# Optimization experiments

Hardware: AMD Instinct MI355X
Metric: run time of the kernel (lower is better)

## Reference

```python
import jax, jax.numpy as jnp
import numpy as np

B, CIN, COUT = 4, 256, 256
H, W = 48, 48
KH = KW = 7
SH = SW = 1
PH = PW = 3
REL = COUT // 2  # rel_size with groups=1


def setup_inputs() -> dict:
    key = jax.random.key(0)
    ks = jax.random.split(key, 7)
    fan = float(CIN)
    x = jax.random.normal(ks[0], (B, CIN, H, W), jnp.float32)
    w_q = jax.random.normal(ks[1], (COUT, CIN), jnp.float32) * (2.0 / fan) ** 0.5
    w_k = jax.random.normal(ks[2], (COUT, CIN), jnp.float32) * (2.0 / fan) ** 0.5
    w_v = jax.random.normal(ks[3], (COUT, CIN), jnp.float32) * (2.0 / fan) ** 0.5
    bound = 1.0 / np.sqrt(COUT)
    bias = jax.random.uniform(ks[4], (1, COUT, 1, 1), jnp.float32, -bound, bound)
    rel_x = jax.random.normal(ks[5], (REL, KW), jnp.float32)
    rel_y = jax.random.normal(ks[6], (COUT - REL, KH), jnp.float32)
    return {"x": x, "w_q": w_q, "w_k": w_k, "w_v": w_v, "bias": bias,
            "rel_x": rel_x, "rel_y": rel_y}


def reference(x, w_q, w_k, w_v, bias, rel_x, rel_y):
    b = x.shape[0]
    ph, pw = H + 2 * PH, W + 2 * PW
    fh = (ph - KH) // SH + 1
    fw = (pw - KW) // SW + 1
    xp = jnp.pad(x, ((0, 0), (0, 0), (PH, PH), (PW, PW)))
    # 1x1 convs (groups=1) as channel matmuls
    vq = jnp.einsum('oc,bchw->bohw', w_q, xp)
    vk = jnp.einsum('oc,bchw->bohw', w_k, xp)
    vv = jnp.einsum('oc,bchw->bohw', w_v, xp)
    # query at window centers: [b, C, fh, fw]
    win_q = vq[:, :, (KH - 1) // 2: ph - KH // 2: SH, (KW - 1) // 2: pw - KW // 2: SW]
    # relative position terms (sum over channel halves)
    qx = jnp.einsum('bxhw,xk->bhwk', win_q[:, :REL], rel_x)        # [b,fh,fw,kw]
    qy = jnp.einsum('byhw,yk->bhwk', win_q[:, REL:], rel_y)        # [b,fh,fw,kh]
    # overlapping windows via gather (equivalent to torch unfold)
    I = jnp.arange(fh)[:, None] * SH + jnp.arange(KH)[None, :]     # [fh,kh]
    J = jnp.arange(fw)[:, None] * SW + jnp.arange(KW)[None, :]     # [fw,kw]
    win_k = vk[:, :, I[:, None, :, None], J[None, :, None, :]]     # [b,C,fh,fw,kh,kw]
    # channel-summed attention logits (shared across channels, as in source)
    scores = jnp.einsum('bchw,bchwkl->bhwkl', win_q, win_k)
    scores = scores + qy[:, :, :, :, None] + qx[:, :, :, None, :]
    attn = jax.nn.softmax(scores.reshape(b, fh, fw, KH * KW), axis=-1)
    attn = attn.reshape(b, fh, fw, KH, KW)
    win_v = vv[:, :, I[:, None, :, None], J[None, :, None, :]]     # [b,C,fh,fw,kh,kw]
    out = jnp.einsum('bhwkl,bchwkl->bchw', attn, win_v) + bias
    return out
```

## Files before the change

kernel.cpp:

```cpp
#include <hip/hip_runtime.h>

#define BB 4
#define CC 256
#define HH 48
#define WW 48
#define HWHW 2304
#define KK 49
#define RELN 128

#define QSZ (BB*CC*HWHW)
#define ATTNOFF (3*QSZ)
#define SBUF_FLOATS (BB*HH*64*WW)
#define WTOFF (ATTNOFF + SBUF_FLOATS)
#define WT_FLOATS 196608
#define KBOFF (WTOFF + WT_FLOATS)
#define KB_FLOATS 3145728
#define RBOFF (KBOFF + KB_FLOATS)

typedef short bf16x8 __attribute__((ext_vector_type(8)));
typedef float f32x4 __attribute__((ext_vector_type(4)));

__device__ __forceinline__ void split_bf16(float f, unsigned short& hi, unsigned short& lo)
{
    unsigned u = __float_as_uint(f);
    hi = (unsigned short)(u >> 16);
    float r = f - __uint_as_float(u & 0xFFFF0000u);
    unsigned v = __float_as_uint(r);
    v += 0x7FFFu + ((v >> 16) & 1u);
    lo = (unsigned short)(v >> 16);
}

__device__ __forceinline__ void gload16(const uint4* g, uint4* l)
{
    __builtin_amdgcn_global_load_lds(
        (const __attribute__((address_space(1))) void*)g,
        (__attribute__((address_space(3))) void*)l, 16, 0, 0);
}

__global__ __launch_bounds__(256) void prep_kernel(
    const float* __restrict__ x,
    const float* __restrict__ wq, const float* __restrict__ wk,
    const float* __restrict__ wvp,
    const float* __restrict__ relx, const float* __restrict__ rely,
    unsigned short* __restrict__ xt, unsigned short* __restrict__ wt,
    float* __restrict__ ws)
{
    __shared__ unsigned short lds[32*520];
    const int bid = blockIdx.x;
    const int t = threadIdx.x;

    if (bid < 288) {
        const int b = bid / 72;
        const int hw0 = (bid % 72) * 32;
        const int hw = t & 31, cp = t >> 5;
        #pragma unroll 4
        for (int i = 0; i < 32; ++i) {
            int c = i*8 + cp;
            float f = x[((size_t)b*CC + c)*HWHW + hw0 + hw];
            unsigned short hi, lo; split_bf16(f, hi, lo);
            int ch = i*2;
            lds[hw*520 + ((ch       ^ (hw&7))*8) + cp] = hi;
            lds[hw*520 + (((ch + 1) ^ (hw&7))*8) + cp] = lo;
        }
        __syncthreads();
        const int hw2 = t >> 3, u = t & 7;
        uint4* xt4 = (uint4*)xt;
        const size_t rowbase = ((size_t)b*HWHW + hw0 + hw2) * 64;
        #pragma unroll
        for (int j = 0; j < 8; ++j) {
            int chunk = j*8 + u;
            uint4 v = *(const uint4*)&lds[hw2*520 + chunk*8];
            xt4[rowbase + chunk] = v;
        }
        return;
    }
    if (bid < 384) {
        const int tt = (bid - 288)*256 + t;
        const int m = tt >> 5, kg = tt & 31;
        const float* src = (m < 256) ? wq : (m < 512) ? wk : wvp;
        const float* row = src + (size_t)(m & 255)*256 + kg*8;
        unsigned short h[8], l[8];
        #pragma unroll
        for (int j = 0; j < 8; ++j) split_bf16(row[j], h[j], l[j]);
        uint4 hv, lv;
        hv.x = (unsigned)h[0] | ((unsigned)h[1]<<16); hv.y = (unsigned)h[2] | ((unsigned)h[3]<<16);
        hv.z = (unsigned)h[4] | ((unsigned)h[5]<<16); hv.w = (unsigned)h[6] | ((unsigned)h[7]<<16);
        lv.x = (unsigned)l[0] | ((unsigned)l[1]<<16); lv.y = (unsigned)l[2] | ((unsigned)l[3]<<16);
        lv.z = (unsigned)l[4] | ((unsigned)l[5]<<16); lv.w = (unsigned)l[6] | ((unsigned)l[7]<<16);
        uint4* dstrow = (uint4*)wt + (size_t)m*64;
        const int ks = kg >> 2, s_hi = 2*(kg & 3);
        dstrow[ks*8 + ( s_hi      ^ (m&7))] = hv;
        dstrow[ks*8 + ((s_hi + 1) ^ (m&7))] = lv;
        return;
    }
    if (bid < 576) {
        uint4* kb4 = (uint4*)(ws + KBOFF);
        const uint4 z = make_uint4(0u,0u,0u,0u);
        int u0 = (bid - 384)*256 + t;
        #pragma unroll
        for (int it = 0; it < 4; ++it) {
            int u = u0 + it*49152;
            int bch = u >> 7, rem = u & 127;
            int r16 = rem >> 3, gr = rem & 7;
            int r = (r16 < 3) ? r16 : 48 + r16;
            kb4[((size_t)bch*64 + r)*8 + gr] = z;
        }
        return;
    }
    {
        unsigned short* rb = (unsigned short*)(ws + RBOFF);
        #pragma unroll
        for (int it = 0; it < 4; ++it) {
            int idx = t + it*256;
            int gi  = idx & 7;
            int l   = (idx >> 3) & 15;
            int ck4 = (idx >> 7) & 3;
            int rel = idx >> 9;
            int isLo = gi >> 2, g4i = gi & 3;
            unsigned short vals[8];
            #pragma unroll
            for (int j = 0; j < 8; ++j) {
                int cl = ck4*32 + g4i*8 + j;
                float f = (l < 7) ? (rel ? rely[cl*7 + l] : relx[cl*7 + l]) : 0.f;
                unsigned short hi, lo; split_bf16(f, hi, lo);
                vals[j] = isLo ? lo : hi;
            }
            int slot = gi ^ (l & 7);
            unsigned short* dst = rb + (((size_t)rel*4 + ck4)*16 + l)*64 + slot*8;
            uint4 pack;
            pack.x = (unsigned)vals[0] | ((unsigned)vals[1]<<16);
            pack.y = (unsigned)vals[2] | ((unsigned)vals[3]<<16);
            pack.z = (unsigned)vals[4] | ((unsigned)vals[5]<<16);
            pack.w = (unsigned)vals[6] | ((unsigned)vals[7]<<16);
            *(uint4*)dst = pack;
        }
    }
}

__global__ __launch_bounds__(256) void proj_gemm_kernel(
    const unsigned short* __restrict__ xt,
    const unsigned short* __restrict__ wt,
    float* __restrict__ ws)
{
    __shared__ uint4 smem[2][1024];
    const int n0 = blockIdx.x * 64;
    const int m0 = blockIdx.y * 64;
    const int b = n0 / HWHW;
    const int hwb = n0 % HWHW;
    const int tid = threadIdx.x;
    const int wid = tid >> 6, ln = tid & 63;
    const int wm = wid >> 1, wn = wid & 1;
    const int l15 = ln & 15, g = ln >> 4;

    f32x4 acc[2][2];
    #pragma unroll
    for (int i = 0; i < 2; ++i)
        #pragma unroll
        for (int j = 0; j < 2; ++j) acc[i][j] = (f32x4){0.f,0.f,0.f,0.f};

    const uint4* wt4 = (const uint4*)wt;
    const uint4* xt4 = (const uint4*)xt;
    const int lrow = ln >> 3, lslot = ln & 7;

    #define STAGE(bf, ks)                                                          \
        {                                                                          \
            _Pragma("unroll")                                                      \
            for (int i = 0; i < 2; ++i) {                                          \
                int seg = wid*2 + i;                                               \
                int row = seg*8 + lrow;                                            \
                gload16(wt4 + (size_t)(m0 + row)*64 + (ks)*8 + lslot,              \
                        &smem[bf][seg*64]);                                        \
                gload16(xt4 + (size_t)(n0 + row)*64 + (ks)*8 + lslot,              \
                        &smem[bf][512 + seg*64]);                                  \
            }                                                                      \
        }

    STAGE(0, 0);
    #pragma unroll
    for (int ks = 0; ks < 8; ++ks) {
        const int cur = ks & 1;
        if (ks < 7) STAGE(cur ^ 1, ks + 1);
        if (ks < 7) asm volatile("s_waitcnt vmcnt(4)" ::: "memory");
        else        asm volatile("s_waitcnt vmcnt(0)" ::: "memory");
        __builtin_amdgcn_s_barrier();
        __builtin_amdgcn_sched_barrier(0);
        bf16x8 aH[2], aL[2], bH[2], bL[2];
        #pragma unroll
        for (int mt = 0; mt < 2; ++mt) {
            int rA = wm*32 + mt*16 + l15;
            aH[mt] = *(const bf16x8*)&smem[cur][rA*8 + ((2*g)   ^ (rA&7))];
            aL[mt] = *(const bf16x8*)&smem[cur][rA*8 + ((2*g+1) ^ (rA&7))];
        }
        #pragma unroll
        for (int nt = 0; nt < 2; ++nt) {
            int rB = wn*32 + nt*16 + l15;
            bH[nt] = *(const bf16x8*)&smem[cur][512 + rB*8 + ((2*g)   ^ (rB&7))];
            bL[nt] = *(const bf16x8*)&smem[cur][512 + rB*8 + ((2*g+1) ^ (rB&7))];
        }
        #pragma unroll
        for (int mt = 0; mt < 2; ++mt)
            #pragma unroll
            for (int nt = 0; nt < 2; ++nt) {
                acc[mt][nt] = __builtin_amdgcn_mfma_f32_16x16x32_bf16(aH[mt], bH[nt], acc[mt][nt], 0, 0, 0);
                acc[mt][nt] = __builtin_amdgcn_mfma_f32_16x16x32_bf16(aH[mt], bL[nt], acc[mt][nt], 0, 0, 0);
                acc[mt][nt] = __builtin_amdgcn_mfma_f32_16x16x32_bf16(aL[mt], bH[nt], acc[mt][nt], 0, 0, 0);
            }
        if (ks < 7) {
            asm volatile("s_waitcnt lgkmcnt(0)" ::: "memory");
            __builtin_amdgcn_s_barrier();
        }
    }
    #undef STAGE

    const int proj = m0 >> 8;
    if (proj == 2) {
        #pragma unroll
        for (int mt = 0; mt < 2; ++mt) {
            int chb = (m0 & 255) + wm*32 + mt*16 + 4*g;
            int ch4 = chb >> 2;
            #pragma unroll
            for (int nt = 0; nt < 2; ++nt) {
                int hw = hwb + wn*32 + nt*16 + l15;
                float* dst = ws + (size_t)2*QSZ + (((size_t)b*64 + ch4)*HWHW + hw)*4;
                *(f32x4*)dst = acc[mt][nt];
            }
        }
        return;
    }
    __syncthreads();
    unsigned short* eb = (unsigned short*)&smem[0][0];
    #pragma unroll
    for (int mt = 0; mt < 2; ++mt) {
        const int chb = (m0 & 255) + wm*32 + mt*16 + 4*g;
        const int ckl = (chb >> 5) & 1;
        const int p = chb & 31, g8 = p >> 3, half = (p >> 2) & 1;
        #pragma unroll
        for (int nt = 0; nt < 2; ++nt) {
            const int hwl = wn*32 + nt*16 + l15;
            const int w = (hwb + hwl) % 48;
            const int key = (proj == 0 ? w : w + 3) & 7;
            f32x4 v = acc[mt][nt];
            unsigned short h0,h1,h2,h3,q0,q1,q2,q3;
            split_bf16(v[0],h0,q0); split_bf16(v[1],h1,q1);
            split_bf16(v[2],h2,q2); split_bf16(v[3],h3,q3);
            uint2 hv, lv;
            hv.x = (unsigned)h0 | ((unsigned)h1<<16); hv.y = (unsigned)h2 | ((unsigned)h3<<16);
            lv.x = (unsigned)q0 | ((unsigned)q1<<16); lv.y = (unsigned)q2 | ((unsigned)q3<<16);
            const int base = (ckl*64 + hwl)*64;
            *(uint2*)(eb + base + ((g8 ^ key)*8 + half*4))     = hv;
            *(uint2*)(eb + base + (((g8+4) ^ key)*8 + half*4)) = lv;
        }
    }
    __syncthreads();
    const int ck0 = (m0 & 255) >> 5;
    if (proj == 0) {
        const uint4* src = (const uint4*)eb;
        uint4* qb4 = (uint4*)ws;
        #pragma unroll
        for (int ckl2 = 0; ckl2 < 2; ++ckl2) {
            uint4* dst = qb4 + (((size_t)b*8 + ck0 + ckl2)*HWHW + hwb)*8;
            #pragma unroll
            for (int it = 0; it < 2; ++it)
                dst[tid + it*256] = src[ckl2*512 + tid + it*256];
        }
    } else {
        uint4* kb4 = (uint4*)(ws + KBOFF);
        const uint4* src = (const uint4*)eb;
        #pragma unroll
        for (int it = 0; it < 4; ++it) {
            int u = tid + it*256;
            int row = u >> 3, gr = u & 7;
            int ckl2 = row >> 6, hwl2 = row & 63;
            int hw2 = hwb + hwl2, h2 = hw2/48, w2 = hw2%48;
            uint4* dst = kb4 + ((((size_t)b*8 + ck0 + ckl2)*48 + h2)*64 + (w2+3))*8;
            dst[gr] = src[u];
        }
    }
}

__global__ __launch_bounds__(512) void scores2_kernel(float* __restrict__ ws)
{
    __shared__ unsigned short sAll[2][4096*8];
    __shared__ float sc[63][48];

    const int bid = blockIdx.x;
    const int b = bid / 48, h = bid % 48;
    const int tid = threadIdx.x;
    const int wv = tid >> 6, ln = tid & 63;
    const int l15 = ln & 15, g4 = ln >> 4;
    const int key = l15 & 7;

    const unsigned short* QB = (const unsigned short*)ws;
    const unsigned short* KB = (const unsigned short*)(ws + KBOFF);
    const unsigned short* RB = (const unsigned short*)(ws + RBOFF);

    for (int u = tid; u < 63*48; u += 512) ((float*)sc)[u] = 0.f;

    const int dk = wv;
    const int hp = h + dk - 3;
    const bool dok = (wv < 7) && (hp >= 0) && (hp < 48);

    f32x4 acc[6], qx[3], qy[3];
    #pragma unroll
    for (int i = 0; i < 6; ++i) acc[i] = (f32x4){0.f,0.f,0.f,0.f};
    #pragma unroll
    for (int i = 0; i < 3; ++i) { qx[i] = (f32x4){0.f,0.f,0.f,0.f}; qy[i] = (f32x4){0.f,0.f,0.f,0.f}; }

    #define SSTAGE(bf, ck)                                                         \
        {                                                                          \
            _Pragma("unroll")                                                      \
            for (int e = 0; e < 8; ++e) {                                          \
                const int I = wv*8 + e;                                            \
                uint4* dst = (uint4*)sAll[bf] + I*64;                              \
                if (I < 6) {                                                       \
                    int unit = I*64 + ln; int row = unit >> 3, gr = unit & 7;      \
                    gload16((const uint4*)QB                                       \
                        + ((((size_t)b*8 + (ck))*48 + h)*48 + row)*8 + gr, dst);   \
                } else if (I < 62) {                                               \
                    int uk = (I-6)*64 + ln;                                        \
                    int kri = uk >> 9;                                             \
                    int wi = uk & 511; int row = wi >> 3, gr = wi & 7;             \
                    int kh = h + kri - 3;                                          \
                    int khc = kh < 0 ? 0 : (kh > 47 ? 47 : kh);                    \
                    gload16((const uint4*)KB                                       \
                        + ((((size_t)b*8 + (ck))*48 + khc)*64 + row)*8 + gr, dst); \
                } else {                                                           \
                    int ur = (I-62)*64 + ln; int row = ur >> 3, gr = ur & 7;       \
                    int rel = (ck) >> 2, c4 = (ck) & 3;                            \
                    gload16((const uint4*)RB                                       \
                        + (((size_t)rel*4 + c4)*16 + row)*8 + gr, dst);            \
                }                                                                  \
            }                                                                      \
        }

    SSTAGE(0, 0);
    for (int ck = 0; ck < 8; ++ck) {
        const int cur = ck & 1;
        if (ck < 7) SSTAGE(cur ^ 1, ck + 1);
        if (ck < 7) asm volatile("s_waitcnt vmcnt(8)" ::: "memory");
        else        asm volatile("s_waitcnt vmcnt(0)" ::: "memory");
        __builtin_amdgcn_s_barrier();
        __builtin_amdgcn_sched_barrier(0);

        const unsigned short* sQ = sAll[cur];
        const unsigned short* sK = sAll[cur] + 384*8;
        const unsigned short* sR = sAll[cur] + 3968*8;

        bf16x8 AH[3], AL[3];
        #pragma unroll
        for (int i = 0; i < 3; ++i) {
            const unsigned short* qr = sQ + (16*i + l15)*64;
            AH[i] = *(const bf16x8*)(qr + ((g4       ^ key)*8));
            AL[i] = *(const bf16x8*)(qr + (((g4 + 4) ^ key)*8));
        }

        if (wv < 7) {
            if (dok) {
                const unsigned short* kbase = sK + dk*4096;
                bf16x8 BH[4], BL[4];
                #pragma unroll
                for (int j = 0; j < 4; ++j) {
                    const unsigned short* kr = kbase + (j*16 + l15)*64;
                    BH[j] = *(const bf16x8*)(kr + ((g4       ^ key)*8));
                    BL[j] = *(const bf16x8*)(kr + (((g4 + 4) ^ key)*8));
                }
                #pragma unroll
                for (int i = 0; i < 3; ++i) {
                    acc[i*2]   = __builtin_amdgcn_mfma_f32_16x16x32_bf16(AH[i], BH[i],   acc[i*2],   0,0,0);
                    acc[i*2]   = __builtin_amdgcn_mfma_f32_16x16x32_bf16(AH[i], BL[i],   acc[i*2],   0,0,0);
                    acc[i*2]   = __builtin_amdgcn_mfma_f32_16x16x32_bf16(AL[i], BH[i],   acc[i*2],   0,0,0);
                    acc[i*2+1] = __builtin_amdgcn_mfma_f32_16x16x32_bf16(AH[i], BH[i+1], acc[i*2+1], 0,0,0);
                    acc[i*2+1] = __builtin_amdgcn_mfma_f32_16x16x32_bf16(AH[i], BL[i+1], acc[i*2+1], 0,0,0);
                    acc[i*2+1] = __builtin_amdgcn_mfma_f32_16x16x32_bf16(AL[i], BH[i+1], acc[i*2+1], 0,0,0);
                }
            }
        } else {
            const unsigned short* rr = sR + l15*64;
            bf16x8 RH = *(const bf16x8*)(rr + ((g4       ^ key)*8));
            bf16x8 RL = *(const bf16x8*)(rr + (((g4 + 4) ^ key)*8));
            if (ck < 4) {
                #pragma unroll
                for (int i = 0; i < 3; ++i) {
                    qx[i] = __builtin_amdgcn_mfma_f32_16x16x32_bf16(AH[i], RH, qx[i], 0,0,0);
                    qx[i] = __builtin_amdgcn_mfma_f32_16x16x32_bf16(AH[i], RL, qx[i], 0,0,0);
                    qx[i] = __builtin_amdgcn_mfma_f32_16x16x32_bf16(AL[i], RH, qx[i], 0,0,0);
                }
            } else {
                #pragma unroll
                for (int i = 0; i < 3; ++i) {
                    qy[i] = __builtin_amdgcn_mfma_f32_16x16x32_bf16(AH[i], RH, qy[i], 0,0,0);
                    qy[i] = __builtin_amdgcn_mfma_f32_16x16x32_bf16(AH[i], RL, qy[i], 0,0,0);
                    qy[i] = __builtin_amdgcn_mfma_f32_16x16x32_bf16(AL[i], RH, qy[i], 0,0,0);
                }
            }
        }
        if (ck < 7) {
            asm volatile("s_waitcnt lgkmcnt(0)" ::: "memory");
            __builtin_amdgcn_s_barrier();
        }
    }
    #undef SSTAGE

    const int n = l15;
    if (wv < 7) {
        if (dok) {
            #pragma unroll
            for (int i = 0; i < 3; ++i)
                #pragma unroll
                for (int a = 0; a < 2; ++a) {
                    f32x4 A = acc[i*2+a];
                    #pragma unroll
                    for (int r = 0; r < 4; ++r) {
                        int m = 4*g4 + r;
                        int dl = n - m + a*16;
                        if (dl >= 0 && dl < 7)
                            sc[dk*7 + dl][16*i + m] = A[r];
                    }
                }
        }
    } else {
        if (n < 7) {
            #pragma unroll
            for (int i = 0; i < 3; ++i)
                #pragma unroll
                for (int r = 0; r < 4; ++r) {
                    sc[49 + n][16*i + 4*g4 + r] = qx[i][r];
                    sc[56 + n][16*i + 4*g4 + r] = qy[i][r];
                }
        }
    }
    __syncthreads();

    if (tid < 48) {
        const int w = tid;
        float tot[KK], rx[7], ry[7];
        #pragma unroll
        for (int i = 0; i < KK; ++i) tot[i] = sc[i][w];
        #pragma unroll
        for (int l = 0; l < 7; ++l) { rx[l] = sc[49+l][w]; ry[l] = sc[56+l][w]; }
        float mx = -1e30f;
        #pragma unroll
        for (int dk2 = 0; dk2 < 7; ++dk2)
            #pragma unroll
            for (int dl = 0; dl < 7; ++dl) {
                tot[dk2*7+dl] += ry[dk2] + rx[dl];
                mx = fmaxf(mx, tot[dk2*7+dl]);
            }
        float sum = 0.f;
        #pragma unroll
        for (int i = 0; i < KK; ++i) { float e = __expf(tot[i]-mx); tot[i]=e; sum += e; }
        float inv = 1.f/sum;
        float* base = ws + ATTNOFF + ((size_t)(b*HH + h)*64)*WW + w;
        #pragma unroll
        for (int i = 0; i < KK; ++i) base[(size_t)i*WW] = tot[i]*inv;
    }
}

__global__ __launch_bounds__(128) void pv_kernel(
    const float* __restrict__ bias,
    const float* __restrict__ ws,
    float* __restrict__ out)
{
    const float* vbuf = ws + (size_t)2*QSZ;
    const float* attn = ws + ATTNOFF;

    const int bid = blockIdx.x;
    const int pxt = bid % 18;
    const int pgq = (bid / 18) % 16;
    const int b   = bid / (18*16);

    const int tid = threadIdx.x;
    const int pxg = tid & 31;
    const int pg  = pgq*4 + (tid >> 5);

    const int hw0 = pxt*128 + pxg*4;
    const int w0 = hw0 % WW;
    const int h0 = hw0 / WW;

    const float* vb = vbuf + ((size_t)b*64 + pg)*HWHW*4;
    const float* ab = attn + ((size_t)(b*HH + h0)*64)*WW;

    const float4 b4 = *(const float4*)(bias + pg*4);
    f32x4 bias4 = (f32x4){b4.x, b4.y, b4.z, b4.w};
    f32x4 acc[4];
    #pragma unroll
    for (int p = 0; p < 4; ++p) acc[p] = bias4;

    #pragma unroll
    for (int dk = 0; dk < 7; ++dk) {
        const int gr = h0 + dk - 3;
        const bool rok = (gr >= 0 && gr < HH);
        f32x4 vrow[10];
        #pragma unroll
        for (int jj = 0; jj < 10; ++jj) {
            const int gc = w0 - 3 + jj;
            vrow[jj] = (rok && gc >= 0 && gc < WW)
                ? *(const f32x4*)(vb + ((size_t)gr*WW + gc)*4)
                : (f32x4){0.f,0.f,0.f,0.f};
        }
        const float* arow = ab + (size_t)(dk*7)*WW + w0;
        #pragma unroll
        for (int dl = 0; dl < 7; ++dl) {
            const float4 av = *(const float4*)(arow + (size_t)dl*WW);
            acc[0] += vrow[dl+0] * av.x;
            acc[1] += vrow[dl+1] * av.y;
            acc[2] += vrow[dl+2] * av.z;
            acc[3] += vrow[dl+3] * av.w;
        }
    }
    #pragma unroll
    for (int c = 0; c < 4; ++c) {
        float4 o;
        o.x = acc[0][c]; o.y = acc[1][c]; o.z = acc[2][c]; o.w = acc[3][c];
        *(float4*)(out + ((size_t)b*CC + pg*4 + c)*HWHW + hw0) = o;
    }
}

extern "C" void kernel_launch(void* const* d_in, const int* in_sizes, int n_in,
                              void* d_out, int out_size, void* d_ws, size_t ws_size,
                              hipStream_t stream) {
    const float* x    = (const float*)d_in[0];
    const float* wq   = (const float*)d_in[1];
    const float* wk   = (const float*)d_in[2];
    const float* wv   = (const float*)d_in[3];
    const float* bias = (const float*)d_in[4];
    const float* relx = (const float*)d_in[5];
    const float* rely = (const float*)d_in[6];
    float* ws  = (float*)d_ws;
    float* out = (float*)d_out;
    unsigned short* xt = (unsigned short*)d_out;
    unsigned short* wt = (unsigned short*)(ws + WTOFF);

    prep_kernel<<<dim3(577), dim3(256), 0, stream>>>(x, wq, wk, wv, relx, rely, xt, wt, ws);
    proj_gemm_kernel<<<dim3(144, 12), dim3(256), 0, stream>>>(xt, wt, ws);
    scores2_kernel<<<dim3(BB*HH), dim3(512), 0, stream>>>(ws);
    pv_kernel<<<dim3(BB*16*18), dim3(128), 0, stream>>>(bias, ws, out);
}
```

Before: 72.44 us.

## Widen projection GEMM tile to 256 output channels per block

The projection GEMM now gives each block all 256 channels of one projection (8 waves, 512 threads) instead of 64, and orders the grid so the three projections of one spatial tile run next to each other. Each X tile is loaded once per projection rather than four times, which cuts global and LDS staging traffic. In exchange the grid shrinks from 1728 to 432 blocks, and each block uses more LDS and registers, so occupancy drops.

```diff
diff --git a/kernel.cpp b/kernel.cpp
--- a/kernel.cpp
+++ b/kernel.cpp
@@ -137,14 +137,14 @@
     }
 }
 
-__global__ __launch_bounds__(256) void proj_gemm_kernel(
+__global__ __launch_bounds__(512) void proj_gemm_kernel(
     const unsigned short* __restrict__ xt,
     const unsigned short* __restrict__ wt,
     float* __restrict__ ws)
 {
-    __shared__ uint4 smem[2][1024];
-    const int n0 = blockIdx.x * 64;
-    const int m0 = blockIdx.y * 64;
+    __shared__ uint4 smem[2][2560];
+    const int m0 = blockIdx.x * 256;
+    const int n0 = blockIdx.y * 64;
     const int b = n0 / HWHW;
     const int hwb = n0 % HWHW;
     const int tid = threadIdx.x;
@@ -152,9 +152,9 @@
     const int wm = wid >> 1, wn = wid & 1;
     const int l15 = ln & 15, g = ln >> 4;
 
-    f32x4 acc[2][2];
-    #pragma unroll
-    for (int i = 0; i < 2; ++i)
+    f32x4 acc[4][2];
+    #pragma unroll
+    for (int i = 0; i < 4; ++i)
         #pragma unroll
         for (int j = 0; j < 2; ++j) acc[i][j] = (f32x4){0.f,0.f,0.f,0.f};
 
@@ -165,13 +165,16 @@
     #define STAGE(bf, ks)                                                          \
         {                                                                          \
             _Pragma("unroll")                                                      \
-            for (int i = 0; i < 2; ++i) {                                          \
-                int seg = wid*2 + i;                                               \
+            for (int i = 0; i < 4; ++i) {                                          \
+                int seg = wid*4 + i;                                               \
                 int row = seg*8 + lrow;                                            \
                 gload16(wt4 + (size_t)(m0 + row)*64 + (ks)*8 + lslot,              \
                         &smem[bf][seg*64]);                                        \
+            }                                                                      \
+            {                                                                      \
+                int row = wid*8 + lrow;                                            \
                 gload16(xt4 + (size_t)(n0 + row)*64 + (ks)*8 + lslot,              \
-                        &smem[bf][512 + seg*64]);                                  \
+                        &smem[bf][2048 + wid*64]);                                 \
             }                                                                      \
         }
 
@@ -180,25 +183,25 @@
     for (int ks = 0; ks < 8; ++ks) {
         const int cur = ks & 1;
         if (ks < 7) STAGE(cur ^ 1, ks + 1);
-        if (ks < 7) asm volatile("s_waitcnt vmcnt(4)" ::: "memory");
+        if (ks < 7) asm volatile("s_waitcnt vmcnt(5)" ::: "memory");
         else        asm volatile("s_waitcnt vmcnt(0)" ::: "memory");
         __builtin_amdgcn_s_barrier();
         __builtin_amdgcn_sched_barrier(0);
-        bf16x8 aH[2], aL[2], bH[2], bL[2];
-        #pragma unroll
-        for (int mt = 0; mt < 2; ++mt) {
-            int rA = wm*32 + mt*16 + l15;
+        bf16x8 aH[4], aL[4], bH[2], bL[2];
+        #pragma unroll
+        for (int mt = 0; mt < 4; ++mt) {
+            int rA = wm*64 + mt*16 + l15;
             aH[mt] = *(const bf16x8*)&smem[cur][rA*8 + ((2*g)   ^ (rA&7))];
             aL[mt] = *(const bf16x8*)&smem[cur][rA*8 + ((2*g+1) ^ (rA&7))];
         }
         #pragma unroll
         for (int nt = 0; nt < 2; ++nt) {
             int rB = wn*32 + nt*16 + l15;
-            bH[nt] = *(const bf16x8*)&smem[cur][512 + rB*8 + ((2*g)   ^ (rB&7))];
-            bL[nt] = *(const bf16x8*)&smem[cur][512 + rB*8 + ((2*g+1) ^ (rB&7))];
-        }
-        #pragma unroll
-        for (int mt = 0; mt < 2; ++mt)
+            bH[nt] = *(const bf16x8*)&smem[cur][2048 + rB*8 + ((2*g)   ^ (rB&7))];
+            bL[nt] = *(const bf16x8*)&smem[cur][2048 + rB*8 + ((2*g+1) ^ (rB&7))];
+        }
+        #pragma unroll
+        for (int mt = 0; mt < 4; ++mt)
             #pragma unroll
             for (int nt = 0; nt < 2; ++nt) {
                 acc[mt][nt] = __builtin_amdgcn_mfma_f32_16x16x32_bf16(aH[mt], bH[nt], acc[mt][nt], 0, 0, 0);
@@ -212,12 +215,11 @@
     }
     #undef STAGE
 
-    const int proj = m0 >> 8;
+    const int proj = blockIdx.x;
     if (proj == 2) {
         #pragma unroll
-        for (int mt = 0; mt < 2; ++mt) {
-            int chb = (m0 & 255) + wm*32 + mt*16 + 4*g;
-            int ch4 = chb >> 2;
+        for (int mt = 0; mt < 4; ++mt) {
+            int ch4 = wm*16 + mt*4 + g;
             #pragma unroll
             for (int nt = 0; nt < 2; ++nt) {
                 int hw = hwb + wn*32 + nt*16 + l15;
@@ -230,9 +232,9 @@
     __syncthreads();
     unsigned short* eb = (unsigned short*)&smem[0][0];
     #pragma unroll
-    for (int mt = 0; mt < 2; ++mt) {
-        const int chb = (m0 & 255) + wm*32 + mt*16 + 4*g;
-        const int ckl = (chb >> 5) & 1;
+    for (int mt = 0; mt < 4; ++mt) {
+        const int chb = wm*64 + mt*16 + 4*g;
+        const int ck = chb >> 5;
         const int p = chb & 31, g8 = p >> 3, half = (p >> 2) & 1;
         #pragma unroll
         for (int nt = 0; nt < 2; ++nt) {
@@ -246,34 +248,30 @@
             uint2 hv, lv;
             hv.x = (unsigned)h0 | ((unsigned)h1<<16); hv.y = (unsigned)h2 | ((unsigned)h3<<16);
             lv.x = (unsigned)q0 | ((unsigned)q1<<16); lv.y = (unsigned)q2 | ((unsigned)q3<<16);
-            const int base = (ckl*64 + hwl)*64;
+            const int base = (ck*64 + hwl)*64;
             *(uint2*)(eb + base + ((g8 ^ key)*8 + half*4))     = hv;
             *(uint2*)(eb + base + (((g8+4) ^ key)*8 + half*4)) = lv;
         }
     }
     __syncthreads();
-    const int ck0 = (m0 & 255) >> 5;
     if (proj == 0) {
         const uint4* src = (const uint4*)eb;
         uint4* qb4 = (uint4*)ws;
         #pragma unroll
-        for (int ckl2 = 0; ckl2 < 2; ++ckl2) {
-            uint4* dst = qb4 + (((size_t)b*8 + ck0 + ckl2)*HWHW + hwb)*8;
-            #pragma unroll
-            for (int it = 0; it < 2; ++it)
-                dst[tid + it*256] = src[ckl2*512 + tid + it*256];
+        for (int ck = 0; ck < 8; ++ck) {
+            uint4* dst = qb4 + (((size_t)b*8 + ck)*HWHW + hwb)*8;
+            dst[tid] = src[ck*512 + tid];
         }
     } else {
         uint4* kb4 = (uint4*)(ws + KBOFF);
         const uint4* src = (const uint4*)eb;
         #pragma unroll
-        for (int it = 0; it < 4; ++it) {
-            int u = tid + it*256;
+        for (int it = 0; it < 8; ++it) {
+            int u = it*512 + tid;
             int row = u >> 3, gr = u & 7;
-            int ckl2 = row >> 6, hwl2 = row & 63;
-            int hw2 = hwb + hwl2, h2 = hw2/48, w2 = hw2%48;
-            uint4* dst = kb4 + ((((size_t)b*8 + ck0 + ckl2)*48 + h2)*64 + (w2+3))*8;
-            dst[gr] = src[u];
+            int ck = row >> 6, hwl = row & 63;
+            int hw2 = hwb + hwl, h2 = hw2/48, w2 = hw2%48;
+            kb4[((((size_t)b*8 + ck)*48 + h2)*64 + (w2+3))*8 + gr] = src[u];
         }
     }
 }
@@ -532,7 +530,7 @@
     unsigned short* wt = (unsigned short*)(ws + WTOFF);
 
     prep_kernel<<<dim3(577), dim3(256), 0, stream>>>(x, wq, wk, wv, relx, rely, xt, wt, ws);
-    proj_gemm_kernel<<<dim3(144, 12), dim3(256), 0, stream>>>(xt, wt, ws);
+    proj_gemm_kernel<<<dim3(3, 144), dim3(512), 0, stream>>>(xt, wt, ws);
     scores2_kernel<<<dim3(BB*HH), dim3(512), 0, stream>>>(ws);
     pv_kernel<<<dim3(BB*16*18), dim3(128), 0, stream>>>(bias, ws, out);
 }
```

Measured after the change: 72.43 us. About the same (-0.0%).
